# Kernel optimization log

Hardware: AMD Instinct MI355X
Metric: run time of the kernel (lower is better)

The kernel has to match this reference:

```python
import jax, jax.numpy as jnp
import numpy as np

N = 50000        # nodes
E = 250000       # edges (avg degree 5)
D = 32           # embed_dim
N_LAYERS = 3


def _uniform(key, shape, fan_in):
    s = 1.0 / np.sqrt(fan_in)
    return jax.random.uniform(key, shape, jnp.float32, -s, s)


def setup_inputs() -> dict:
    key = jax.random.key(0)
    ks = jax.random.split(key, 10)
    x = jax.random.normal(ks[0], (N, 1), jnp.float32)
    edge_index = jax.random.randint(ks[1], (2, E), 0, N, dtype=jnp.int64)
    edge_attribute = jax.random.normal(ks[2], (E, 1), jnp.float32)
    # Linear weights stored as [in, out] (i.e. torch weight transposed)
    node_W = _uniform(ks[3], (1, D), 1)
    node_b = _uniform(ks[4], (D,), 1)
    l1_W = _uniform(ks[5], (1, D * D), 1)
    l1_b = _uniform(ks[6], (D * D,), 1)
    root = _uniform(ks[7], (D, D), D)      # NNConv root weight
    conv_b = _uniform(ks[8], (D,), D)      # NNConv bias
    return {
        "x": x, "edge_index": edge_index, "edge_attribute": edge_attribute,
        "i": 2, "dummy": 0,
        "node_W": node_W, "node_b": node_b,
        "l1_W": l1_W, "l1_b": l1_b,
        "root": root, "conv_b": conv_b,
    }


def reference(x, edge_index, edge_attribute, i, dummy, node_W, node_b,
              l1_W, l1_b, root, conv_b):
    n_encode_layers = min(i + 1, N_LAYERS)
    src, dst = edge_index[0], edge_index[1]

    # node embedding: [N,1] -> [N,D]
    h = x @ node_W + node_b

    # edge-conditioned weight matrices, shared by every layer: [E, D, D]
    We = (edge_attribute @ l1_W + l1_b).reshape(E, D, D)

    # mean-aggregation denominator (in-degree, clamped; isolated nodes -> 0 msg)
    cnt = jax.ops.segment_sum(jnp.ones((E,), h.dtype), dst, num_segments=N)
    cnt = jnp.maximum(cnt, 1.0)[:, None]

    for _ in range(n_encode_layers):
        h = jax.nn.relu(h)
        # gather source features, per-edge matmul: msg_e = x_src[e] @ We[e]
        msg = jnp.einsum('ei,eio->eo', h[src], We)
        aggr = jax.ops.segment_sum(msg, dst, num_segments=N) / cnt
        h = aggr + h @ root + conv_b
    return h
```

## Files before the change

kernel.cpp:

```cpp
#include <hip/hip_runtime.h>
#include <hip/hip_bf16.h>

#define N_NODES 50000
#define N_EDGES 250000
#define DIM 32
#define BLK 256
#define CAP 32
#define SPILL_MAX 4096
#define EDGE_NB 977
#define WCONV_NB 13
#define LAYER_NB 1563
#define POISON 0xAAAAAAAAu

typedef __attribute__((ext_vector_type(8))) short short8;
typedef __attribute__((ext_vector_type(4))) float f32x4;

__device__ __forceinline__ float ldf(const void* p, int i, int isf32) {
    return isf32 ? ((const float*)p)[i]
                 : __bfloat162float(((const __hip_bfloat16*)p)[i]);
}
__device__ __forceinline__ int ldi(const int* ei, int i, int i64) {
    return i64 ? ei[2 * i] : ei[i];
}
__device__ __forceinline__ int clamp_idx(int v) {
    v = v < 0 ? 0 : v;
    return v >= N_NODES ? N_NODES - 1 : v;
}
__device__ __forceinline__ bool half_is_big(const void* p, int k) {
    unsigned short h = ((const unsigned short*)p)[k];
    float v = __uint_as_float(((unsigned int)h) << 16);
    return !(fabsf(v) <= 50.0f);
}
__device__ __forceinline__ unsigned short bf16bits(float v) {
    __hip_bfloat16 b = __float2bfloat16(v);
    return __builtin_bit_cast(unsigned short, b);
}

__global__ __launch_bounds__(BLK) void prep_kernel(
    const int* __restrict__ ei, const void* __restrict__ ea,
    const void* __restrict__ lW, const void* __restrict__ lb,
    const void* __restrict__ rt, const void* __restrict__ cb,
    int* __restrict__ cntI, int2* __restrict__ packed,
    int* __restrict__ spill_cnt, int4* __restrict__ spill,
    float* __restrict__ wCB, unsigned short* __restrict__ wfrag)
{
    __shared__ int sdet;
    int tid = threadIdx.x;
    int b = blockIdx.x;
    if (tid == 0) sdet = 0;
    __syncthreads();

    if (b < EDGE_NB) {
        if (tid < 64) {
            if (ei[2 * tid + 1] != 0) atomicOr(&sdet, 2);
        } else if (tid < 192) {
            if (half_is_big(ea, tid - 64)) atomicOr(&sdet, 1);
        }
        __syncthreads();
        int f_ea = sdet & 1, i64 = ((sdet & 2) == 0);
        int e = b * BLK + tid;
        if (e < N_EDGES) {
            int s = clamp_idx(ldi(ei, e, i64));
            int d = clamp_idx(ldi(ei, N_EDGES + e, i64));
            float a = ldf(ea, e, f_ea);
            unsigned k = (unsigned)atomicAdd(&cntI[d], 1) - POISON;
            if (k < CAP) {
                packed[d * CAP + (int)k] = make_int2(s, __float_as_int(a));
            } else {
                unsigned sp = (unsigned)atomicAdd(spill_cnt, 1) - POISON;
                if (sp < SPILL_MAX)
                    spill[sp] = make_int4(d, s, __float_as_int(a), 0);
            }
        }
        return;
    }

    if (tid < 64)       { if (half_is_big(lW, tid) || half_is_big(lW, tid + 64)) atomicOr(&sdet, 1); }
    else if (tid < 128) { int k = tid - 64;  if (half_is_big(lb, k) || half_is_big(lb, k + 64)) atomicOr(&sdet, 2); }
    else if (tid < 192) { int k = tid - 128; if (half_is_big(rt, k) || half_is_big(rt, k + 64)) atomicOr(&sdet, 4); }
    else if (tid < 224) { if (half_is_big(cb, tid - 192)) atomicOr(&sdet, 8); }
    __syncthreads();
    int fW = sdet & 1, fB = sdet & 2, fR = sdet & 4, fC = sdet & 8;
    int g = (int)(b - EDGE_NB) * BLK + tid;
    if (g < 3072) {
        int f = g >> 9, rem = g & 511;
        int ln = rem >> 3, j = rem & 7;
        int t = f >> 1, nh = f & 1;
        int k = t * 32 + (ln >> 4) * 8 + j;
        int n = nh * 16 + (ln & 15);
        float v;
        if (k < 32)      v = ldf(lW, k * 32 + n, fW);
        else if (k < 64) v = ldf(lb, (k - 32) * 32 + n, fB);
        else             v = ldf(rt, (k - 64) * 32 + n, fR);
        wfrag[g] = bf16bits(v);
    } else if (g < 3104) {
        wCB[g - 3072] = ldf(cb, g - 3072, fC);
    }
}

__global__ __launch_bounds__(512) void layer_kernel(
    const int2* __restrict__ packed, const int* __restrict__ cntI,
    const int* __restrict__ spill_cnt, const int4* __restrict__ spill,
    const void* __restrict__ x, const void* __restrict__ nW,
    const void* __restrict__ nb,
    const float* __restrict__ hin, const float* __restrict__ wCB,
    const unsigned short* __restrict__ wfrag,
    float* __restrict__ outb, int mode0, int last)
{
    __shared__ __align__(16) unsigned short sAu[32 * 96];
    __shared__ int sdet;
    int tid = threadIdx.x;
    int wv = tid >> 6;
    int lane = tid & 63;
    int half = lane >> 5;
    int l32 = lane & 31;
    int nbase = blockIdx.x * 32;
    int n0 = nbase + wv * 4;

    float nWl = 0.0f, nbl = 0.0f;
    int f_x = 0;
    if (mode0) {
        if (tid == 0) sdet = 0;
        __syncthreads();
        if (tid < 128) {
            if (half_is_big(x, tid)) atomicOr(&sdet, 4);
        } else if (tid < 160) {
            if (half_is_big(nW, tid - 128)) atomicOr(&sdet, 8);
        } else if (tid < 192) {
            if (half_is_big(nb, tid - 160)) atomicOr(&sdet, 16);
        }
        __syncthreads();
        f_x = sdet & 4;
        nWl = ldf(nW, l32, sdet & 8);
        nbl = ldf(nb, l32, sdet & 16);
    }

    int deg[4];
    #pragma unroll
    for (int j = 0; j < 4; ++j) {
        int n = n0 + j;
        deg[j] = (n < N_NODES) ? (int)((unsigned)cntI[n] - POISON) : 0;
    }

    float hl01, hl23;
    if (mode0) {
        int na = clamp_idx(n0 + half), nc = clamp_idx(n0 + 2 + half);
        float xa = ldf(x, na, f_x), xc = ldf(x, nc, f_x);
        hl01 = fmaf(xa, nWl, nbl); hl01 = hl01 > 0.0f ? hl01 : 0.0f;
        hl23 = fmaf(xc, nWl, nbl); hl23 = hl23 > 0.0f ? hl23 : 0.0f;
    } else {
        hl01 = hin[n0 * DIM + lane];
        hl23 = hin[(n0 + 2) * DIM + lane];
    }

    int2 c[4][4];
    #pragma unroll
    for (int j = 0; j < 4; ++j) {
        int base = (n0 + j) * CAP;
        #pragma unroll
        for (int i = 0; i < 4; ++i)
            c[j][i] = packed[base + 2 * i + half];
    }
    float h[4][4];
    #pragma unroll
    for (int j = 0; j < 4; ++j) {
        #pragma unroll
        for (int i = 0; i < 4; ++i) {
            int src = ((2 * i + half) < deg[j]) ? c[j][i].x : 0;
            if (mode0) {
                float xs = ldf(x, src, f_x);
                float hv = fmaf(xs, nWl, nbl);
                h[j][i] = hv > 0.0f ? hv : 0.0f;
            } else {
                h[j][i] = hin[src * DIM + l32];
            }
        }
    }
    float p[4] = {0, 0, 0, 0}, q[4] = {0, 0, 0, 0};
    #pragma unroll
    for (int j = 0; j < 4; ++j) {
        #pragma unroll
        for (int i = 0; i < 4; ++i) {
            bool valid = (2 * i + half) < deg[j];
            float hv = valid ? h[j][i] : 0.0f;
            float a  = valid ? __int_as_float(c[j][i].y) : 0.0f;
            p[j] = fmaf(a, hv, p[j]);
            q[j] += hv;
        }
    }
    #pragma unroll
    for (int j = 0; j < 4; ++j) {
        int dgc = deg[j] < CAP ? deg[j] : CAP;
        for (int k = 8 + half; k < dgc; k += 2) {
            int2 cc = packed[(n0 + j) * CAP + k];
            float hv;
            if (mode0) {
                float xs = ldf(x, cc.x, f_x);
                hv = fmaf(xs, nWl, nbl);
                hv = hv > 0.0f ? hv : 0.0f;
            } else {
                hv = hin[cc.x * DIM + l32];
            }
            p[j] = fmaf(__int_as_float(cc.y), hv, p[j]);
            q[j] += hv;
        }
    }
    unsigned spt = (unsigned)(*spill_cnt) - POISON;
    if (spt != 0) {
        if (spt > SPILL_MAX) spt = SPILL_MAX;
        #pragma unroll
        for (int j = 0; j < 4; ++j) {
            if (deg[j] > CAP) {
                for (unsigned t = (unsigned)half; t < spt; t += 2) {
                    int4 sp = spill[t];
                    if (sp.x == n0 + j) {
                        float hv;
                        if (mode0) {
                            float xs = ldf(x, sp.y, f_x);
                            hv = fmaf(xs, nWl, nbl);
                            hv = hv > 0.0f ? hv : 0.0f;
                        } else {
                            hv = hin[sp.y * DIM + l32];
                        }
                        p[j] = fmaf(__int_as_float(sp.z), hv, p[j]);
                        q[j] += hv;
                    }
                }
            }
        }
    }
    #pragma unroll
    for (int j = 0; j < 4; ++j) {
        p[j] += __shfl_xor(p[j], 32);
        q[j] += __shfl_xor(q[j], 32);
        float ic = 1.0f / (deg[j] < 1 ? 1.0f : (float)deg[j]);
        p[j] *= ic;
        q[j] *= ic;
    }
    #pragma unroll
    for (int j = 0; j < 4; ++j)
        sAu[(wv * 4 + j) * 96 + half * 32 + l32] = bf16bits(half ? q[j] : p[j]);
    sAu[(wv * 4 + half) * 96 + 64 + l32] = bf16bits(hl01);
    sAu[(wv * 4 + 2 + half) * 96 + 64 + l32] = bf16bits(hl23);
    __syncthreads();

    if (wv < 4) {
        int rg = wv & 1, nh = wv >> 1;
        short8 bfr[3];
        #pragma unroll
        for (int t = 0; t < 3; ++t)
            bfr[t] = *(const short8*)(wfrag + ((t * 2 + nh) * 64 + lane) * 8);
        f32x4 acc = {0.0f, 0.0f, 0.0f, 0.0f};
        #pragma unroll
        for (int t = 0; t < 3; ++t) {
            short8 afr = *(const short8*)(sAu + (rg * 16 + (lane & 15)) * 96
                                          + t * 32 + (lane >> 4) * 8);
            acc = __builtin_amdgcn_mfma_f32_16x16x32_bf16(afr, bfr[t], acc, 0, 0, 0);
        }
        float cbl = wCB[nh * 16 + (lane & 15)];
        #pragma unroll
        for (int r = 0; r < 4; ++r) {
            int row = rg * 16 + (lane >> 4) * 4 + r;
            int n = nbase + row;
            if (n < N_NODES) {
                float v = acc[r] + cbl;
                if (!last) v = v > 0.0f ? v : 0.0f;
                outb[n * DIM + nh * 16 + (lane & 15)] = v;
            }
        }
    }
}

extern "C" void kernel_launch(void* const* d_in, const int* in_sizes, int n_in,
                              void* d_out, int out_size, void* d_ws, size_t ws_size,
                              hipStream_t stream) {
    const void* p[16];
    int np_ = 0;
    for (int i = 0; i < n_in && np_ < 16; ++i)
        if (in_sizes[i] != 1) p[np_++] = d_in[i];

    const void* x      = p[0];
    const int*  ei     = (const int*)p[1];
    const void* ea     = p[2];
    const void* node_W = p[3];
    const void* node_b = p[4];
    const void* l1_W   = p[5];
    const void* l1_b   = p[6];
    const void* root   = p[7];
    const void* conv_b = p[8];
    float* out = (float*)d_out;

    const int ND = N_NODES * DIM;
    float* ws = (float*)d_ws;
    int2*  packed    = (int2*)ws;
    float* hr1       = (float*)(packed + N_NODES * CAP);
    float* hr2       = hr1 + ND;
    float* wCB       = hr2 + ND;
    unsigned short* wfrag = (unsigned short*)(wCB + 32);
    int*   cntI      = (int*)(wfrag + 3072);
    int*   spill_cnt = cntI + N_NODES;
    int4*  spill     = (int4*)(spill_cnt + 3);

    prep_kernel<<<EDGE_NB + WCONV_NB, BLK, 0, stream>>>(
        ei, ea, l1_W, l1_b, root, conv_b,
        cntI, packed, spill_cnt, spill, wCB, wfrag);

    layer_kernel<<<LAYER_NB, 512, 0, stream>>>(packed, cntI, spill_cnt, spill,
        x, node_W, node_b, hr2 , wCB, wfrag, hr1, 1, 0);
    layer_kernel<<<LAYER_NB, 512, 0, stream>>>(packed, cntI, spill_cnt, spill,
        x, node_W, node_b, hr1, wCB, wfrag, hr2, 0, 0);
    layer_kernel<<<LAYER_NB, 512, 0, stream>>>(packed, cntI, spill_cnt, spill,
        x, node_W, node_b, hr2, wCB, wfrag, out, 0, 1);
}
```

Baseline: 148.7 us.

## Fuse prep and three layer kernels into one cooperative persistent kernel

Replaces the prep kernel and three layer launches with a single cooperative kernel of 512 persistent blocks. Grid-wide syncs separate the CSR build from each layer, and each block loops over node tiles. This removes three kernel launch gaps and their tail effects. In exchange, every layer pays for grid-wide barriers, occupancy is capped by the co-residency limit, and the old multi-kernel path remains as a fallback if the cooperative launch fails.

Measured after the change: 350.5 us. 2.36x slower.

```diff
diff --git a/kernel.cpp b/kernel.cpp
--- a/kernel.cpp
+++ b/kernel.cpp
@@ -1,5 +1,8 @@
 #include <hip/hip_runtime.h>
 #include <hip/hip_bf16.h>
+#include <hip/hip_cooperative_groups.h>
+
+namespace cg = cooperative_groups;
 
 #define N_NODES 50000
 #define N_EDGES 250000
@@ -10,6 +13,7 @@
 #define EDGE_NB 977
 #define WCONV_NB 13
 #define LAYER_NB 1563
+#define GRID 512
 #define POISON 0xAAAAAAAAu
 
 typedef __attribute__((ext_vector_type(8))) short short8;
@@ -34,6 +38,253 @@
 __device__ __forceinline__ unsigned short bf16bits(float v) {
     __hip_bfloat16 b = __float2bfloat16(v);
     return __builtin_bit_cast(unsigned short, b);
+}
+
+__global__ __launch_bounds__(512, 4) void fused_kernel(
+    const int* __restrict__ ei, const void* __restrict__ ea,
+    const void* __restrict__ lW, const void* __restrict__ lb,
+    const void* __restrict__ rt, const void* __restrict__ cb,
+    const void* __restrict__ x, const void* __restrict__ nW,
+    const void* __restrict__ nb,
+    int2* __restrict__ packed, int* __restrict__ cntI,
+    int* __restrict__ spill_cnt, int4* __restrict__ spill,
+    float* __restrict__ wCB, unsigned short* __restrict__ wfrag,
+    float* __restrict__ hr1, float* __restrict__ hr2,
+    float* __restrict__ out)
+{
+    __shared__ __align__(16) unsigned short sAu[32 * 96];
+    __shared__ int sdet;
+    cg::grid_group gg = cg::this_grid();
+
+    int tid = threadIdx.x;
+    int b = blockIdx.x;
+    int wv = tid >> 6;
+    int lane = tid & 63;
+    int half = lane >> 5;
+    int l32 = lane & 31;
+
+    if (tid == 0) sdet = 0;
+    __syncthreads();
+    if (tid < 64) {
+        if (ei[2 * tid + 1] != 0) atomicOr(&sdet, 2);
+        if (half_is_big(rt, tid) || half_is_big(rt, tid + 64)) atomicOr(&sdet, 128);
+    } else if (tid < 192) {
+        if (half_is_big(ea, tid - 64)) atomicOr(&sdet, 1);
+    } else if (tid < 320) {
+        if (half_is_big(x, tid - 192)) atomicOr(&sdet, 4);
+    } else if (tid < 352) {
+        if (half_is_big(nW, tid - 320)) atomicOr(&sdet, 8);
+        if (half_is_big(cb, tid - 320)) atomicOr(&sdet, 256);
+    } else if (tid < 384) {
+        if (half_is_big(nb, tid - 352)) atomicOr(&sdet, 16);
+    } else if (tid < 448) {
+        int k = tid - 384;
+        if (half_is_big(lW, k) || half_is_big(lW, k + 64)) atomicOr(&sdet, 32);
+    } else {
+        int k = tid - 448;
+        if (half_is_big(lb, k) || half_is_big(lb, k + 64)) atomicOr(&sdet, 64);
+    }
+    __syncthreads();
+    int det = sdet;
+    int f_ea = det & 1, i64 = ((det & 2) == 0), f_x = det & 4;
+
+    {
+        int e = b * 512 + tid;
+        if (e < N_EDGES) {
+            int s = clamp_idx(ldi(ei, e, i64));
+            int d = clamp_idx(ldi(ei, N_EDGES + e, i64));
+            float a = ldf(ea, e, f_ea);
+            unsigned k = (unsigned)atomicAdd(&cntI[d], 1) - POISON;
+            if (k < CAP) {
+                packed[d * CAP + (int)k] = make_int2(s, __float_as_int(a));
+            } else {
+                unsigned sp = (unsigned)atomicAdd(spill_cnt, 1) - POISON;
+                if (sp < SPILL_MAX)
+                    spill[sp] = make_int4(d, s, __float_as_int(a), 0);
+            }
+        }
+    }
+    {
+        int g = b * 512 + tid;
+        if (g < 3072) {
+            int f = g >> 9, rem = g & 511;
+            int ln = rem >> 3, j = rem & 7;
+            int t = f >> 1, nh = f & 1;
+            int k = t * 32 + (ln >> 4) * 8 + j;
+            int n = nh * 16 + (ln & 15);
+            float v;
+            if (k < 32)      v = ldf(lW, k * 32 + n, det & 32);
+            else if (k < 64) v = ldf(lb, (k - 32) * 32 + n, det & 64);
+            else             v = ldf(rt, (k - 64) * 32 + n, det & 128);
+            wfrag[g] = bf16bits(v);
+        } else if (g < 3104) {
+            wCB[g - 3072] = ldf(cb, g - 3072, det & 256);
+        }
+    }
+
+    float nWl = ldf(nW, l32, det & 8);
+    float nbl = ldf(nb, l32, det & 16);
+
+    gg.sync();
+
+    short8 bfr[3];
+    {
+        int nh = (wv >> 1) & 1;
+        #pragma unroll
+        for (int t = 0; t < 3; ++t)
+            bfr[t] = *(const short8*)(wfrag + ((t * 2 + nh) * 64 + lane) * 8);
+    }
+    float cbl = wCB[((wv >> 1) & 1) * 16 + (lane & 15)];
+
+    #pragma unroll 1
+    for (int l = 0; l < 3; ++l) {
+        const float* hin = (l == 1) ? hr1 : hr2;
+        float* outb = (l == 0) ? hr1 : (l == 1) ? hr2 : out;
+        int mode0 = (l == 0);
+        int last = (l == 2);
+        unsigned spt = (unsigned)(*spill_cnt) - POISON;
+        if (spt > SPILL_MAX) spt = SPILL_MAX;
+
+        for (int unit = b; unit < LAYER_NB; unit += GRID) {
+            int nbase = unit * 32;
+            int n0 = nbase + wv * 4;
+
+            int deg[4];
+            #pragma unroll
+            for (int j = 0; j < 4; ++j) {
+                int n = n0 + j;
+                deg[j] = (n < N_NODES) ? (int)((unsigned)cntI[n] - POISON) : 0;
+            }
+
+            float hl01, hl23;
+            if (mode0) {
+                int na = clamp_idx(n0 + half), nc = clamp_idx(n0 + 2 + half);
+                float xa = ldf(x, na, f_x), xc = ldf(x, nc, f_x);
+                hl01 = fmaf(xa, nWl, nbl); hl01 = hl01 > 0.0f ? hl01 : 0.0f;
+                hl23 = fmaf(xc, nWl, nbl); hl23 = hl23 > 0.0f ? hl23 : 0.0f;
+            } else {
+                hl01 = hin[n0 * DIM + lane];
+                hl23 = hin[(n0 + 2) * DIM + lane];
+            }
+
+            int2 c[4][4];
+            #pragma unroll
+            for (int j = 0; j < 4; ++j) {
+                int base = (n0 + j) * CAP;
+                #pragma unroll
+                for (int i = 0; i < 4; ++i)
+                    c[j][i] = packed[base + 2 * i + half];
+            }
+            float h[4][4];
+            #pragma unroll
+            for (int j = 0; j < 4; ++j) {
+                #pragma unroll
+                for (int i = 0; i < 4; ++i) {
+                    int src = ((2 * i + half) < deg[j]) ? c[j][i].x : 0;
+                    if (mode0) {
+                        float xs = ldf(x, src, f_x);
+                        float hv = fmaf(xs, nWl, nbl);
+                        h[j][i] = hv > 0.0f ? hv : 0.0f;
+                    } else {
+                        h[j][i] = hin[src * DIM + l32];
+                    }
+                }
+            }
+            float p[4] = {0, 0, 0, 0}, q[4] = {0, 0, 0, 0};
+            #pragma unroll
+            for (int j = 0; j < 4; ++j) {
+                #pragma unroll
+                for (int i = 0; i < 4; ++i) {
+                    bool valid = (2 * i + half) < deg[j];
+                    float hv = valid ? h[j][i] : 0.0f;
+                    float a  = valid ? __int_as_float(c[j][i].y) : 0.0f;
+                    p[j] = fmaf(a, hv, p[j]);
+                    q[j] += hv;
+                }
+            }
+            #pragma unroll
+            for (int j = 0; j < 4; ++j) {
+                int dgc = deg[j] < CAP ? deg[j] : CAP;
+                for (int k = 8 + half; k < dgc; k += 2) {
+                    int2 cc = packed[(n0 + j) * CAP + k];
+                    float hv;
+                    if (mode0) {
+                        float xs = ldf(x, cc.x, f_x);
+                        hv = fmaf(xs, nWl, nbl);
+                        hv = hv > 0.0f ? hv : 0.0f;
+                    } else {
+                        hv = hin[cc.x * DIM + l32];
+                    }
+                    p[j] = fmaf(__int_as_float(cc.y), hv, p[j]);
+                    q[j] += hv;
+                }
+            }
+            if (spt != 0) {
+                #pragma unroll
+                for (int j = 0; j < 4; ++j) {
+                    if (deg[j] > CAP) {
+                        for (unsigned t = (unsigned)half; t < spt; t += 2) {
+                            int4 sp = spill[t];
+                            if (sp.x == n0 + j) {
+                                float hv;
+                                if (mode0) {
+                                    float xs = ldf(x, sp.y, f_x);
+                                    hv = fmaf(xs, nWl, nbl);
+                                    hv = hv > 0.0f ? hv : 0.0f;
+                                } else {
+                                    hv = hin[sp.y * DIM + l32];
+                                }
+                                p[j] = fmaf(__int_as_float(sp.z), hv, p[j]);
+                                q[j] += hv;
+                            }
+                        }
+                    }
+                }
+            }
+            #pragma unroll
+            for (int j = 0; j < 4; ++j) {
+                p[j] += __shfl_xor(p[j], 32);
+                q[j] += __shfl_xor(q[j], 32);
+                float ic = 1.0f / (deg[j] < 1 ? 1.0f : (float)deg[j]);
+                p[j] *= ic;
+                q[j] *= ic;
+            }
+
+            __syncthreads();
+            #pragma unroll
+            for (int j = 0; j < 4; ++j)
+                sAu[(wv * 4 + j) * 96 + half * 32 + l32] =
+                    bf16bits(half ? q[j] : p[j]);
+            sAu[(wv * 4 + half) * 96 + 64 + l32] = bf16bits(hl01);
+            sAu[(wv * 4 + 2 + half) * 96 + 64 + l32] = bf16bits(hl23);
+            __syncthreads();
+
+            if (wv < 4) {
+                int rg = wv & 1;
+                int nh = wv >> 1;
+                f32x4 acc = {0.0f, 0.0f, 0.0f, 0.0f};
+                #pragma unroll
+                for (int t = 0; t < 3; ++t) {
+                    short8 afr = *(const short8*)(sAu
+                        + (rg * 16 + (lane & 15)) * 96
+                        + t * 32 + (lane >> 4) * 8);
+                    acc = __builtin_amdgcn_mfma_f32_16x16x32_bf16(
+                              afr, bfr[t], acc, 0, 0, 0);
+                }
+                #pragma unroll
+                for (int r = 0; r < 4; ++r) {
+                    int row = rg * 16 + (lane >> 4) * 4 + r;
+                    int n = nbase + row;
+                    if (n < N_NODES) {
+                        float v = acc[r] + cbl;
+                        if (!last) v = v > 0.0f ? v : 0.0f;
+                        outb[n * DIM + nh * 16 + (lane & 15)] = v;
+                    }
+                }
+            }
+        }
+        if (l < 2) gg.sync();
+    }
 }
 
 __global__ __launch_bounds__(BLK) void prep_kernel(
@@ -299,16 +550,26 @@
     unsigned short* wfrag = (unsigned short*)(wCB + 32);
     int*   cntI      = (int*)(wfrag + 3072);
     int*   spill_cnt = cntI + N_NODES;
-    int4*  spill     = (int4*)(spill_cnt + 3);
-
-    prep_kernel<<<EDGE_NB + WCONV_NB, BLK, 0, stream>>>(
-        ei, ea, l1_W, l1_b, root, conv_b,
-        cntI, packed, spill_cnt, spill, wCB, wfrag);
-
-    layer_kernel<<<LAYER_NB, 512, 0, stream>>>(packed, cntI, spill_cnt, spill,
-        x, node_W, node_b, hr2 , wCB, wfrag, hr1, 1, 0);
-    layer_kernel<<<LAYER_NB, 512, 0, stream>>>(packed, cntI, spill_cnt, spill,
-        x, node_W, node_b, hr1, wCB, wfrag, hr2, 0, 0);
-    layer_kernel<<<LAYER_NB, 512, 0, stream>>>(packed, cntI, spill_cnt, spill,
-        x, node_W, node_b, hr2, wCB, wfrag, out, 0, 1);
-}
+    int4*  spill     = (int4*)(spill_cnt + 4);
+
+    void* args[] = {
+        (void*)&ei, (void*)&ea, (void*)&l1_W, (void*)&l1_b, (void*)&root,
+        (void*)&conv_b, (void*)&x, (void*)&node_W, (void*)&node_b,
+        (void*)&packed, (void*)&cntI, (void*)&spill_cnt, (void*)&spill,
+        (void*)&wCB, (void*)&wfrag, (void*)&hr1, (void*)&hr2, (void*)&out
+    };
+    hipError_t err = hipLaunchCooperativeKernel(
+        (const void*)fused_kernel, dim3(GRID), dim3(512), args, 0, stream);
+
+    if (err != hipSuccess) {
+        prep_kernel<<<EDGE_NB + WCONV_NB, BLK, 0, stream>>>(
+            ei, ea, l1_W, l1_b, root, conv_b,
+            cntI, packed, spill_cnt, spill, wCB, wfrag);
+        layer_kernel<<<LAYER_NB, 512, 0, stream>>>(packed, cntI, spill_cnt, spill,
+            x, node_W, node_b, hr2 , wCB, wfrag, hr1, 1, 0);
+        layer_kernel<<<LAYER_NB, 512, 0, stream>>>(packed, cntI, spill_cnt, spill,
+            x, node_W, node_b, hr1, wCB, wfrag, hr2, 0, 0);
+        layer_kernel<<<LAYER_NB, 512, 0, stream>>>(packed, cntI, spill_cnt, spill,
+            x, node_W, node_b, hr2, wCB, wfrag, out, 0, 1);
+    }
+}
```

## Store intermediate layer activations as bf16 and vectorize degree loads

Applied to the files above, without the earlier changes.

Intermediate hidden states between layers are now written and gathered as bf16 instead of fp32, halving the bytes moved by the random-access source gathers and the output stores of the first two layers. The final layer still writes fp32. Per-wave degree counts are also read with a single int4 load when all four nodes are in range. The cost is lower precision in the intermediate activations, which could raise numerical error against the fp32 reference.

After: 159.1 us. 1.07x slower.

```diff
diff --git a/kernel.cpp b/kernel.cpp
--- a/kernel.cpp
+++ b/kernel.cpp
@@ -18,6 +18,9 @@
 __device__ __forceinline__ float ldf(const void* p, int i, int isf32) {
     return isf32 ? ((const float*)p)[i]
                  : __bfloat162float(((const __hip_bfloat16*)p)[i]);
+}
+__device__ __forceinline__ float b2f(unsigned short u) {
+    return __uint_as_float(((unsigned int)u) << 16);
 }
 __device__ __forceinline__ int ldi(const int* ei, int i, int i64) {
     return i64 ? ei[2 * i] : ei[i];
@@ -103,9 +106,9 @@
     const int* __restrict__ spill_cnt, const int4* __restrict__ spill,
     const void* __restrict__ x, const void* __restrict__ nW,
     const void* __restrict__ nb,
-    const float* __restrict__ hin, const float* __restrict__ wCB,
+    const unsigned short* __restrict__ hin, const float* __restrict__ wCB,
     const unsigned short* __restrict__ wfrag,
-    float* __restrict__ outb, int mode0, int last)
+    void* __restrict__ outb, int mode0, int last)
 {
     __shared__ __align__(16) unsigned short sAu[32 * 96];
     __shared__ int sdet;
@@ -136,10 +139,18 @@
     }
 
     int deg[4];
-    #pragma unroll
-    for (int j = 0; j < 4; ++j) {
-        int n = n0 + j;
-        deg[j] = (n < N_NODES) ? (int)((unsigned)cntI[n] - POISON) : 0;
+    if (n0 + 3 < N_NODES) {
+        int4 d4 = *(const int4*)(cntI + n0);
+        deg[0] = (int)((unsigned)d4.x - POISON);
+        deg[1] = (int)((unsigned)d4.y - POISON);
+        deg[2] = (int)((unsigned)d4.z - POISON);
+        deg[3] = (int)((unsigned)d4.w - POISON);
+    } else {
+        #pragma unroll
+        for (int j = 0; j < 4; ++j) {
+            int n = n0 + j;
+            deg[j] = (n < N_NODES) ? (int)((unsigned)cntI[n] - POISON) : 0;
+        }
     }
 
     float hl01, hl23;
@@ -149,8 +160,8 @@
         hl01 = fmaf(xa, nWl, nbl); hl01 = hl01 > 0.0f ? hl01 : 0.0f;
         hl23 = fmaf(xc, nWl, nbl); hl23 = hl23 > 0.0f ? hl23 : 0.0f;
     } else {
-        hl01 = hin[n0 * DIM + lane];
-        hl23 = hin[(n0 + 2) * DIM + lane];
+        hl01 = b2f(hin[n0 * DIM + lane]);
+        hl23 = b2f(hin[(n0 + 2) * DIM + lane]);
     }
 
     int2 c[4][4];
@@ -172,7 +183,7 @@
                 float hv = fmaf(xs, nWl, nbl);
                 h[j][i] = hv > 0.0f ? hv : 0.0f;
             } else {
-                h[j][i] = hin[src * DIM + l32];
+                h[j][i] = b2f(hin[src * DIM + l32]);
             }
         }
     }
@@ -199,7 +210,7 @@
                 hv = fmaf(xs, nWl, nbl);
                 hv = hv > 0.0f ? hv : 0.0f;
             } else {
-                hv = hin[cc.x * DIM + l32];
+                hv = b2f(hin[cc.x * DIM + l32]);
             }
             p[j] = fmaf(__int_as_float(cc.y), hv, p[j]);
             q[j] += hv;
@@ -220,7 +231,7 @@
                             hv = fmaf(xs, nWl, nbl);
                             hv = hv > 0.0f ? hv : 0.0f;
                         } else {
-                            hv = hin[sp.y * DIM + l32];
+                            hv = b2f(hin[sp.y * DIM + l32]);
                         }
                         p[j] = fmaf(__int_as_float(sp.z), hv, p[j]);
                         q[j] += hv;
@@ -264,8 +275,13 @@
             int n = nbase + row;
             if (n < N_NODES) {
                 float v = acc[r] + cbl;
-                if (!last) v = v > 0.0f ? v : 0.0f;
-                outb[n * DIM + nh * 16 + (lane & 15)] = v;
+                if (!last) {
+                    v = v > 0.0f ? v : 0.0f;
+                    ((unsigned short*)outb)[n * DIM + nh * 16 + (lane & 15)] =
+                        bf16bits(v);
+                } else {
+                    ((float*)outb)[n * DIM + nh * 16 + (lane & 15)] = v;
+                }
             }
         }
     }
@@ -291,15 +307,15 @@
     float* out = (float*)d_out;
 
     const int ND = N_NODES * DIM;
-    float* ws = (float*)d_ws;
+    char* ws = (char*)d_ws;
     int2*  packed    = (int2*)ws;
-    float* hr1       = (float*)(packed + N_NODES * CAP);
-    float* hr2       = hr1 + ND;
-    float* wCB       = hr2 + ND;
+    unsigned short* hr1 = (unsigned short*)(packed + N_NODES * CAP);
+    unsigned short* hr2 = hr1 + ND;
+    float* wCB       = (float*)(hr2 + ND);
     unsigned short* wfrag = (unsigned short*)(wCB + 32);
     int*   cntI      = (int*)(wfrag + 3072);
     int*   spill_cnt = cntI + N_NODES;
-    int4*  spill     = (int4*)(spill_cnt + 3);
+    int4*  spill     = (int4*)(spill_cnt + 4);
 
     prep_kernel<<<EDGE_NB + WCONV_NB, BLK, 0, stream>>>(
         ei, ea, l1_W, l1_b, root, conv_b,
```
